# Performance work log

Measured on AMD Instinct MI355X. Metric: run time of the kernel, lower is better.

The kernel has to match this reference:

```python
import jax, jax.numpy as jnp
import numpy as np

EPS = 1e-10   # eps added inside cumprod, as in _compute_weights
FAR = 1e10    # last delta, as in forward()
NEAR_D, FAR_D = 2.0, 6.0  # typical NeRF near/far bounds for depth sampling

N_RAYS, N_PTS = 65536, 128


def setup_inputs() -> dict:
    key = jax.random.key(0)
    k1, k2, k3 = jax.random.split(key, 3)
    # densities are non-negative (raw sigma output after relu/softplus)
    density = jax.random.uniform(k1, (N_RAYS, N_PTS), dtype=jnp.float32) * 2.0
    feature = jax.random.uniform(k2, (N_RAYS, N_PTS, 3), dtype=jnp.float32)
    # monotonically increasing sample depths along each ray in [NEAR_D, FAR_D]
    depth_values = jnp.sort(
        jax.random.uniform(k3, (N_RAYS, N_PTS), dtype=jnp.float32,
                           minval=NEAR_D, maxval=FAR_D), axis=-1)
    return {"density": density, "feature": feature, "depth_values": depth_values}


def reference(density, feature, depth_values):
    # deltas: diff of sample depths, last delta = 1e10  -> [N, P]
    deltas = jnp.concatenate(
        [depth_values[..., 1:] - depth_values[..., :-1],
         jnp.full_like(depth_values[..., :1], FAR)], axis=-1)
    alpha = 1.0 - jnp.exp(-deltas * density)                      # [N, P]
    # transmittance: cumprod(1-alpha+eps) rolled right with T[...,0]=1
    Tinc = jnp.cumprod(1.0 - alpha + EPS, axis=-1)                # [N, P]
    T = jnp.concatenate([jnp.ones_like(Tinc[..., :1]), Tinc[..., :-1]], axis=-1)
    weights = T * alpha                                           # [N, P]
    # weighted feature (rgb) and depth aggregation over samples
    rgb = jnp.einsum('np,npc->nc', weights, feature)              # [N, 3]
    depth = jnp.einsum('np,npc->nc', weights,
                       jnp.broadcast_to(depth_values[..., None], feature.shape))  # [N, 3]
    return rgb, depth
```

## Files before the change

### kernel.cpp

```cpp
#include <hip/hip_runtime.h>

#define N_PTS 128
#define EPS_F 1e-10f
#define FAR_F 1e10f

template<int CTRL, int ROW_MASK>
__device__ __forceinline__ float dpp_mov(float src, float old) {
    union { float f; int i; } s, o, r;
    s.f = src; o.f = old;
    r.i = __builtin_amdgcn_update_dpp(o.i, s.i, CTRL, ROW_MASK, 0xF, false);
    return r.f;
}

__device__ __forceinline__ float half32_reduce_add(float x) {
    x += dpp_mov<0x111, 0xF>(x, 0.0f);
    x += dpp_mov<0x112, 0xF>(x, 0.0f);
    x += dpp_mov<0x114, 0xF>(x, 0.0f);
    x += dpp_mov<0x118, 0xF>(x, 0.0f);
    x += dpp_mov<0x142, 0xA>(x, 0.0f);
    return x;
}

__global__ __launch_bounds__(256) void volrend_kernel(
        const float* __restrict__ density,
        const float* __restrict__ feature,
        const float* __restrict__ depth,
        float* __restrict__ out, int n_rays) {
    const int lane = threadIdx.x & 63;
    const int hl   = lane & 31;
    const int half = lane >> 5;
    const int wave0  = (blockIdx.x * blockDim.x + threadIdx.x) >> 6;
    const int nwaves = (gridDim.x * blockDim.x) >> 6;
    const int npairs = n_rays >> 1;

    int p = wave0;
    if (p >= npairs) return;

    int ray = p * 2 + half;
    float4 dns = ((const float4*)(density + (size_t)ray * N_PTS))[hl];
    float4 z   = ((const float4*)(depth   + (size_t)ray * N_PTS))[hl];
    const float4* fp0 = (const float4*)(feature + (size_t)ray * (N_PTS * 3));
    float4 fa = fp0[hl * 3 + 0];
    float4 fb = fp0[hl * 3 + 1];
    float4 fc = fp0[hl * 3 + 2];

    while (true) {
        const int pn = p + nwaves;
        const bool have_next = (pn < npairs);

        float4 dns2, z2, fa2, fb2, fc2;
        if (have_next) {
            const int rayn = pn * 2 + half;
            dns2 = ((const float4*)(density + (size_t)rayn * N_PTS))[hl];
            z2   = ((const float4*)(depth   + (size_t)rayn * N_PTS))[hl];
            const float4* fpn = (const float4*)(feature + (size_t)rayn * (N_PTS * 3));
            fa2 = fpn[hl * 3 + 0];
            fb2 = fpn[hl * 3 + 1];
            fc2 = fpn[hl * 3 + 2];
        }

        float nz = dpp_mov<0x130, 0xF>(z.x, 0.0f);
        float d0 = z.y - z.x;
        float d1 = z.z - z.y;
        float d2 = z.w - z.z;
        float d3 = (hl == 31) ? FAR_F : (nz - z.w);

        float e0 = __expf(-d0 * dns.x), e1 = __expf(-d1 * dns.y);
        float e2 = __expf(-d2 * dns.z), e3 = __expf(-d3 * dns.w);
        float f0 = e0 + EPS_F, f1 = e1 + EPS_F, f2 = e2 + EPS_F, f3 = e3 + EPS_F;
        float a0 = 1.0f - e0,  a1 = 1.0f - e1,  a2 = 1.0f - e2,  a3 = 1.0f - e3;

        float pr = (f0 * f1) * (f2 * f3);
        pr *= dpp_mov<0x111, 0xF>(pr, 1.0f);
        pr *= dpp_mov<0x112, 0xF>(pr, 1.0f);
        pr *= dpp_mov<0x114, 0xF>(pr, 1.0f);
        pr *= dpp_mov<0x118, 0xF>(pr, 1.0f);
        pr *= dpp_mov<0x142, 0xA>(pr, 1.0f);
        float T0 = dpp_mov<0x138, 0xF>(pr, 1.0f);
        T0 = (hl == 0) ? 1.0f : T0;

        float w0 = T0 * a0; float T1 = T0 * f0;
        float w1 = T1 * a1; float T2 = T1 * f1;
        float w2 = T2 * a2; float T3 = T2 * f2;
        float w3 = T3 * a3;

        float rx = half32_reduce_add(w0 * fa.x + w1 * fa.w + w2 * fb.z + w3 * fc.y);
        float ry = half32_reduce_add(w0 * fa.y + w1 * fb.x + w2 * fb.w + w3 * fc.z);
        float rz = half32_reduce_add(w0 * fa.z + w1 * fb.y + w2 * fc.x + w3 * fc.w);
        float dd = half32_reduce_add(w0 * z.x  + w1 * z.y  + w2 * z.z  + w3 * z.w);

        if (hl == 31) {
            float* o  = out + (size_t)ray * 3;
            o[0] = rx; o[1] = ry; o[2] = rz;
            float* od = out + (size_t)n_rays * 3 + (size_t)ray * 3;
            od[0] = dd; od[1] = dd; od[2] = dd;
        }

        if (!have_next) break;
        p   = pn;
        ray = p * 2 + half;
        dns = dns2; z = z2; fa = fa2; fb = fb2; fc = fc2;
    }
}

extern "C" void kernel_launch(void* const* d_in, const int* in_sizes, int n_in,
                              void* d_out, int out_size, void* d_ws, size_t ws_size,
                              hipStream_t stream) {
    const float* density = (const float*)d_in[0];
    const float* feature = (const float*)d_in[1];
    const float* depth   = (const float*)d_in[2];
    float* out = (float*)d_out;
    const int n_rays = in_sizes[0] / N_PTS;
    const int blocks = 1024;
    volrend_kernel<<<blocks, 256, 0, stream>>>(density, feature, depth, out, n_rays);
}
```

Before: 194.9 us.

## Stage per-wave ray-pair inputs into LDS via async global_load_lds double buffering

Replaces the register prefetch of the next ray pair with direct global-to-LDS async loads (global_load_lds, 16 bytes per lane) into a per-wave double buffer. A vmcnt wait lets the current buffer complete while the next pair's loads stay in flight. The aim is to cut the vector registers held by the prefetched float4s and keep more memory requests outstanding. In exchange it adds 40 KB of LDS per block, which may limit occupancy, plus extra LDS reads and a dependence on hand-placed waitcnt and sched_barrier ordering.

```diff
diff --git a/kernel.cpp b/kernel.cpp
--- a/kernel.cpp
+++ b/kernel.cpp
@@ -1,8 +1,13 @@
 #include <hip/hip_runtime.h>
 
-#define N_PTS 128
-#define EPS_F 1e-10f
-#define FAR_F 1e10f
+#define N_PTS   128
+#define EPS_F   1e-10f
+#define FAR_F   1e10f
+#define PAIR_B  5120
+#define WAITCNT_VM(n) (0x0F70 | (n))
+
+typedef const __attribute__((address_space(1))) unsigned int* gptr_t;
+typedef __attribute__((address_space(3))) unsigned int* lptr_t;
 
 template<int CTRL, int ROW_MASK>
 __device__ __forceinline__ float dpp_mov(float src, float old) {
@@ -21,43 +26,64 @@
     return x;
 }
 
+__device__ __forceinline__ void stage_pair(const char* density, const char* feature,
+                                           const char* depth, long long p,
+                                           char* buf, int lane) {
+    const long long lo = (long long)lane * 16;
+    __builtin_amdgcn_global_load_lds((gptr_t)(density + p * 1024 + lo),        (lptr_t)(buf       ), 16, 0, 0);
+    __builtin_amdgcn_global_load_lds((gptr_t)(depth   + p * 1024 + lo),        (lptr_t)(buf + 1024), 16, 0, 0);
+    __builtin_amdgcn_global_load_lds((gptr_t)(feature + p * 3072 + lo),        (lptr_t)(buf + 2048), 16, 0, 0);
+    __builtin_amdgcn_global_load_lds((gptr_t)(feature + p * 3072 + 1024 + lo), (lptr_t)(buf + 3072), 16, 0, 0);
+    __builtin_amdgcn_global_load_lds((gptr_t)(feature + p * 3072 + 2048 + lo), (lptr_t)(buf + 4096), 16, 0, 0);
+}
+
 __global__ __launch_bounds__(256) void volrend_kernel(
         const float* __restrict__ density,
         const float* __restrict__ feature,
         const float* __restrict__ depth,
         float* __restrict__ out, int n_rays) {
+    __shared__ char lds_raw[4 * 2 * PAIR_B];
     const int lane = threadIdx.x & 63;
     const int hl   = lane & 31;
     const int half = lane >> 5;
+    const int wid  = threadIdx.x >> 6;
+    char* const wbase = lds_raw + wid * (2 * PAIR_B);
+
     const int wave0  = (blockIdx.x * blockDim.x + threadIdx.x) >> 6;
     const int nwaves = (gridDim.x * blockDim.x) >> 6;
     const int npairs = n_rays >> 1;
 
+    const char* dsrc = (const char*)density;
+    const char* fsrc = (const char*)feature;
+    const char* zsrc = (const char*)depth;
+
     int p = wave0;
     if (p >= npairs) return;
 
-    int ray = p * 2 + half;
-    float4 dns = ((const float4*)(density + (size_t)ray * N_PTS))[hl];
-    float4 z   = ((const float4*)(depth   + (size_t)ray * N_PTS))[hl];
-    const float4* fp0 = (const float4*)(feature + (size_t)ray * (N_PTS * 3));
-    float4 fa = fp0[hl * 3 + 0];
-    float4 fb = fp0[hl * 3 + 1];
-    float4 fc = fp0[hl * 3 + 2];
+    char* cur = wbase;
+    char* nxt = wbase + PAIR_B;
+    stage_pair(dsrc, fsrc, zsrc, p, cur, lane);
 
     while (true) {
         const int pn = p + nwaves;
         const bool have_next = (pn < npairs);
+        if (have_next) {
+            stage_pair(dsrc, fsrc, zsrc, pn, nxt, lane);
+            __builtin_amdgcn_sched_barrier(0);
+            __builtin_amdgcn_s_waitcnt(WAITCNT_VM(5));
+            __builtin_amdgcn_sched_barrier(0);
+        } else {
+            __builtin_amdgcn_sched_barrier(0);
+            __builtin_amdgcn_s_waitcnt(WAITCNT_VM(0));
+            __builtin_amdgcn_sched_barrier(0);
+        }
 
-        float4 dns2, z2, fa2, fb2, fc2;
-        if (have_next) {
-            const int rayn = pn * 2 + half;
-            dns2 = ((const float4*)(density + (size_t)rayn * N_PTS))[hl];
-            z2   = ((const float4*)(depth   + (size_t)rayn * N_PTS))[hl];
-            const float4* fpn = (const float4*)(feature + (size_t)rayn * (N_PTS * 3));
-            fa2 = fpn[hl * 3 + 0];
-            fb2 = fpn[hl * 3 + 1];
-            fc2 = fpn[hl * 3 + 2];
-        }
+        const float4 dns = *(const float4*)(cur        + half * 512  + hl * 16);
+        const float4 z   = *(const float4*)(cur + 1024 + half * 512  + hl * 16);
+        const char*  fpb = cur + 2048 + half * 1536 + hl * 48;
+        const float4 fa  = *(const float4*)(fpb);
+        const float4 fb  = *(const float4*)(fpb + 16);
+        const float4 fc  = *(const float4*)(fpb + 32);
 
         float nz = dpp_mov<0x130, 0xF>(z.x, 0.0f);
         float d0 = z.y - z.x;
@@ -89,6 +115,7 @@
         float rz = half32_reduce_add(w0 * fa.z + w1 * fb.y + w2 * fc.x + w3 * fc.w);
         float dd = half32_reduce_add(w0 * z.x  + w1 * z.y  + w2 * z.z  + w3 * z.w);
 
+        const int ray = p * 2 + half;
         if (hl == 31) {
             float* o  = out + (size_t)ray * 3;
             o[0] = rx; o[1] = ry; o[2] = rz;
@@ -97,9 +124,8 @@
         }
 
         if (!have_next) break;
-        p   = pn;
-        ray = p * 2 + half;
-        dns = dns2; z = z2; fa = fa2; fb = fb2; fc = fc2;
+        p = pn;
+        char* t = cur; cur = nxt; nxt = t;
     }
 }
 
```

After: 195.1 us. No clear change (+0.1%).
